# Kernel optimization log

Hardware: AMD Instinct MI355X
Metric: run time of the kernel (lower is better)

The kernel has to match this reference:

```python
import math
import jax, jax.numpy as jnp
import numpy as np

B, NPC, K, D, T, L = 512, 32, 12, 64, 64, 4  # crystals, atoms/crystal, knn, node_dim, time_dim, layers
N = B * NPC
E_IN = 2 * D + 1 + T   # 193
N_IN = 2 * D + T       # 192


def setup_inputs() -> dict:
    key = jax.random.key(0)
    ks = jax.random.split(key, 32)
    rn = lambda k, shp, s=0.05: jax.random.normal(k, shp, jnp.float32) * s
    inp = {}
    inp["z_nodes"] = jax.random.normal(ks[0], (N, 128), jnp.float32)
    inp["t"] = jax.random.uniform(ks[1], (B,), jnp.float32) * 1000.0
    inp["frac_coords"] = jax.random.uniform(ks[2], (N, 3), jnp.float32)
    inp["lattice"] = jnp.eye(3, dtype=jnp.float32) * 5.0 + rn(ks[3], (B, 3, 3), 0.3)
    inp["batch_indices"] = jnp.repeat(jnp.arange(B, dtype=jnp.int32), NPC)
    inp["num_atoms"] = NPC
    # time_mlp: Linear(T, 2T) -> SiLU -> Linear(2T, T)
    inp["time_w1"] = rn(ks[4], (T, 2 * T)); inp["time_b1"] = rn(ks[5], (2 * T,))
    inp["time_w2"] = rn(ks[6], (2 * T, T)); inp["time_b2"] = rn(ks[7], (T,))
    # node_embedding: Linear(128, D)
    inp["emb_w"] = rn(ks[8], (128, D)); inp["emb_b"] = rn(ks[9], (D,))
    # per-layer EGNN params stacked on leading L axis
    inp["edge_w1"] = rn(ks[10], (L, E_IN, D)); inp["edge_b1"] = rn(ks[11], (L, D))
    inp["edge_w2"] = rn(ks[12], (L, D, D));    inp["edge_b2"] = rn(ks[13], (L, D))
    inp["coord_w1"] = rn(ks[14], (L, D, D));   inp["coord_b1"] = rn(ks[15], (L, D))
    inp["coord_w2"] = rn(ks[16], (L, D, 1))
    inp["node_w1"] = rn(ks[17], (L, N_IN, D)); inp["node_b1"] = rn(ks[18], (L, D))
    inp["node_w2"] = rn(ks[19], (L, D, D));    inp["node_b2"] = rn(ks[20], (L, D))
    return inp


def _forward(z_nodes, t, frac_coords, lattice, batch_indices, num_atoms,
             time_w1, time_b1, time_w2, time_b2, emb_w, emb_b,
             edge_w1, edge_b1, edge_w2, edge_b2, coord_w1, coord_b1, coord_w2,
             node_w1, node_b1, node_w2, node_b2):
    silu = jax.nn.silu
    n = num_atoms
    b = lattice.shape[0]
    n_nodes = z_nodes.shape[0]

    # ---- time embedding ----
    half = T // 2
    freqs = jnp.exp(jnp.arange(half, dtype=jnp.float32) * (-math.log(10000.0) / (half - 1)))
    ang = t[:, None] * freqs[None, :]
    sinu = jnp.concatenate([jnp.sin(ang), jnp.cos(ang)], axis=-1)  # [B, T]
    t_feat = silu(sinu @ time_w1 + time_b1) @ time_w2 + time_b2     # [B, T]
    t_nodes = t_feat[batch_indices]                                  # [N, T]

    h = z_nodes @ emb_w + emb_b                                      # [N, D]

    # ---- vectorized PBC KNN graph (all crystals have n atoms) ----
    f = frac_coords.reshape(b, n, 3)
    diff_f = f[:, :, None, :] - f[:, None, :, :]
    diff_f = diff_f - jnp.round(diff_f)
    diff_c = jnp.einsum('bijk,bkl->bijl', diff_f, lattice)           # [b,n,n,3]
    dist_sq = jnp.sum(diff_c * diff_c, axis=-1)                      # [b,n,n]
    dist_sq = jnp.where(jnp.eye(n, dtype=bool)[None], jnp.inf, dist_sq)
    k = min(K, n - 1)
    _, idx = jax.lax.top_k(-dist_sq, k)                              # [b,n,k] neighbor indices
    offs = (jnp.arange(b, dtype=jnp.int32) * n)[:, None, None]
    edge_src = (idx + offs).reshape(-1)                              # neighbors j
    edge_dst = (jnp.broadcast_to(jnp.arange(n, dtype=jnp.int32)[None, :, None], (b, n, k)) + offs).reshape(-1)
    diff_cart = jnp.take_along_axis(diff_c, jnp.broadcast_to(idx[..., None], (b, n, k, 3)), axis=2).reshape(-1, 3)
    dist_sq_e = jnp.take_along_axis(dist_sq, idx, axis=2).reshape(-1, 1)

    t_edges = t_nodes[edge_src]                                      # [E, T]

    total_shift = jnp.zeros((n_nodes, 3), dtype=h.dtype)
    for l in range(L):
        edge_in = jnp.concatenate([h[edge_src], h[edge_dst], dist_sq_e, t_edges], axis=-1)
        m = silu(edge_in @ edge_w1[l] + edge_b1[l])
        m = silu(m @ edge_w2[l] + edge_b2[l])                        # [E, D]
        cw = silu(m @ coord_w1[l] + coord_b1[l]) @ coord_w2[l]       # [E, 1]
        coord_update = jax.ops.segment_sum(diff_cart * cw, edge_src, num_segments=n_nodes)
        m_i = jax.ops.segment_sum(m, edge_dst, num_segments=n_nodes)
        node_in = jnp.concatenate([h, m_i, t_nodes], axis=-1)
        h = h + (silu(node_in @ node_w1[l] + node_b1[l]) @ node_w2[l] + node_b2[l])
        total_shift = total_shift + coord_update

    inv_lat = jnp.linalg.inv(lattice)[batch_indices]                 # [N,3,3]
    shift_frac = jnp.einsum('ni,nij->nj', total_shift, inv_lat)
    return shift_frac, h


def reference(z_nodes, t, frac_coords, lattice, batch_indices, num_atoms,
              time_w1, time_b1, time_w2, time_b2, emb_w, emb_b,
              edge_w1, edge_b1, edge_w2, edge_b2, coord_w1, coord_b1, coord_w2,
              node_w1, node_b1, node_w2, node_b2):
    return _forward(z_nodes, t, frac_coords, lattice, batch_indices, num_atoms,
                    time_w1, time_b1, time_w2, time_b2, emb_w, emb_b,
                    edge_w1, edge_b1, edge_w2, edge_b2, coord_w1, coord_b1, coord_w2,
                    node_w1, node_b1, node_w2, node_b2)
```

## Files before the change

### kernel.cpp

```cpp
#include <hip/hip_runtime.h>
#include <hip/hip_bf16.h>
#include <math.h>

#define NB 512
#define NPC 32
#define KNN 12
#define NL 4
#define NN (NB*NPC)
#define WPL 28672

typedef float v4f __attribute__((ext_vector_type(4)));
typedef short s8v __attribute__((ext_vector_type(8)));

__device__ __forceinline__ float silu_f(float x) {
    return x * __builtin_amdgcn_rcpf(1.0f + __builtin_amdgcn_exp2f(x * -1.44269504088896341f));
}

__device__ __forceinline__ unsigned short f2bf(float x) {
    unsigned u = __float_as_uint(x);
    u += 0x7fffu + ((u >> 16) & 1u);
    return (unsigned short)(u >> 16);
}

__device__ __forceinline__ unsigned pk2bf(float a, float b) {
    __hip_bfloat162 t = __float22bfloat162_rn(make_float2(a, b));
    union { __hip_bfloat162 h; unsigned u; } c; c.h = t;
    return c.u;
}

__device__ __forceinline__ int div12(int e) { return (e * 1366) >> 14; }

template<int R>
__device__ __forceinline__ void gemm_acc(const float* A, int astride,
                                         const float* __restrict__ Wg,
                                         int K, int lane, float* acc) {
#pragma unroll 2
    for (int kq = 0; kq < (K >> 2); ++kq) {
        float w0 = Wg[(4*kq+0)*64 + lane];
        float w1 = Wg[(4*kq+1)*64 + lane];
        float w2 = Wg[(4*kq+2)*64 + lane];
        float w3 = Wg[(4*kq+3)*64 + lane];
#pragma unroll
        for (int r = 0; r < R; ++r) {
            float4 a = *(const float4*)(A + r*astride + 4*kq);
            acc[r] = fmaf(a.x, w0, acc[r]);
            acc[r] = fmaf(a.y, w1, acc[r]);
            acc[r] = fmaf(a.z, w2, acc[r]);
            acc[r] = fmaf(a.w, w3, acc[r]);
        }
    }
}

extern "C" __global__ void prepack_w(const float* __restrict__ edge_w1, const float* __restrict__ edge_w2,
                                     const float* __restrict__ coord_w1, const float* __restrict__ node_w1,
                                     const float* __restrict__ node_w2, unsigned short* __restrict__ wout) {
    int g = blockIdx.x * 256 + threadIdx.x;
    if (g >= 4 * WPL / 8) return;
    int l = (g * 8) / WPL;
    int r = (g * 8) % WPL;
    int base, nKt, mat;
    if      (r < 8192)  { base = 0;     nKt = 2; mat = 0; }
    else if (r < 12288) { base = 8192;  nKt = 2; mat = 1; }
    else if (r < 16384) { base = 12288; nKt = 2; mat = 2; }
    else if (r < 24576) { base = 16384; nKt = 4; mat = 3; }
    else                { base = 24576; nKt = 2; mat = 4; }
    int idx = r - base;
    int lane = (idx >> 3) & 63, t = idx >> 9;
    int kt = t % nKt, nt = t / nKt;
    int k0 = kt*32 + ((lane >> 4) & 3)*8;
    int n  = nt*16 + (lane & 15);
    unsigned short o[8];
#pragma unroll
    for (int j = 0; j < 8; ++j) {
        int k = k0 + j;
        float v;
        if      (mat == 0) v = (n < 64) ? edge_w1[l*193*64 + k*64 + n] : edge_w1[l*193*64 + (64+k)*64 + (n-64)];
        else if (mat == 1) v = edge_w2 [l*4096 + k*64 + n];
        else if (mat == 2) v = coord_w1[l*4096 + k*64 + n];
        else if (mat == 3) v = node_w1 [l*192*64 + k*64 + n];
        else               v = node_w2 [l*4096 + k*64 + n];
        o[j] = f2bf(v);
    }
    *(s8v*)(wout + g*8) = *(s8v*)o;
}

extern "C" __global__ __launch_bounds__(512, 2)
void crystal_fused(const float* __restrict__ z_nodes, const float* __restrict__ t_in,
                   const float* __restrict__ frac,    const float* __restrict__ lattice,
                   const float* __restrict__ time_w1, const float* __restrict__ time_b1,
                   const float* __restrict__ time_w2, const float* __restrict__ time_b2,
                   const float* __restrict__ emb_w,   const float* __restrict__ emb_b,
                   const float* __restrict__ edge_w1, const float* __restrict__ edge_b1,
                   const float* __restrict__ edge_b2, const float* __restrict__ coord_b1,
                   const float* __restrict__ coord_w2,
                   const float* __restrict__ node_w1, const float* __restrict__ node_b1,
                   const float* __restrict__ node_b2,
                   const unsigned short* __restrict__ wbf,
                   float* __restrict__ out)
{
    __shared__ __align__(16) float s_h[32*65];
    __shared__ __align__(16) unsigned short s_habf[32*136];
    __shared__ __align__(16) unsigned short s_n1bf[32*72];
    __shared__ __align__(16) float s_hs[32*68];
    __shared__ __align__(16) float s_hd[32*68];
    __shared__ __align__(16) unsigned short s_tiles16[8*1152];
    __shared__ float s_dsq[32][33];
    __shared__ float2 s_emeta[384];
    __shared__ float s_endc[384*3];
    __shared__ float s_frac[32][3];
    __shared__ float s_lat[9], s_inv[9];
    __shared__ float s_sinu[64], s_t1[128], s_tf[64];
    __shared__ float s_tb4[NL*64], s_nb4[NL*64];
    __shared__ float s_shift[32*3];

    const int tid  = threadIdx.x;
    const int c    = blockIdx.x;
    const int lane = tid & 63;
    const int wave = tid >> 6;
    const int q4   = lane >> 4;
    const int c16  = lane & 15;
    const int base = c * NPC;

    if (tid < 96) {
        ((float*)s_frac)[tid] = frac[base*3 + tid];
    } else if (tid < 105) {
        s_lat[tid-96] = lattice[c*9 + (tid-96)];
    } else if (tid >= 128 && tid < 160) {
        int i = tid - 128;
        float freq = expf((float)i * (-9.210340371976184f / 31.0f));
        float ang  = t_in[c] * freq;
        s_sinu[i]    = sinf(ang);
        s_sinu[i+32] = cosf(ang);
    }
    __syncthreads();

    float* dcf = (float*)s_tiles16;
    {
        float l00=s_lat[0],l01=s_lat[1],l02=s_lat[2];
        float l10=s_lat[3],l11=s_lat[4],l12=s_lat[5];
        float l20=s_lat[6],l21=s_lat[7],l22=s_lat[8];
        for (int p = tid; p < 1024; p += 512) {
            int i = p >> 5, j = p & 31;
            float dx = s_frac[i][0]-s_frac[j][0];
            float dy = s_frac[i][1]-s_frac[j][1];
            float dz = s_frac[i][2]-s_frac[j][2];
            dx -= rintf(dx); dy -= rintf(dy); dz -= rintf(dz);
            float cx = dx*l00 + dy*l10 + dz*l20;
            float cy = dx*l01 + dy*l11 + dz*l21;
            float cz = dx*l02 + dy*l12 + dz*l22;
            float dd = cx*cx + cy*cy + cz*cz;
            s_dsq[i][j] = (i==j) ? 3.0e38f : dd;
            dcf[p*3+0]=cx; dcf[p*3+1]=cy; dcf[p*3+2]=cz;
        }
    }
    __syncthreads();

    if (tid < 32) {
        int i = tid;
        for (int k = 0; k < KNN; ++k) {
            float best = 3.9e38f; int bj = 0;
            for (int j = 0; j < 32; ++j) {
                float v = s_dsq[i][j];
                if (v < best) { best = v; bj = j; }
            }
            s_dsq[i][bj] = 3.9e38f;
            int e = i*KNN + k;
            s_emeta[e] = make_float2(best, __int_as_float(bj));
            int p = (i<<5) + bj;
            s_endc[e*3+0] = dcf[p*3+0];
            s_endc[e*3+1] = dcf[p*3+1];
            s_endc[e*3+2] = dcf[p*3+2];
        }
    } else if (tid >= 128 && tid < 256) {
        int jj = tid - 128;
        float p0 = time_b1[jj], p1=0.f, p2=0.f, p3=0.f;
        for (int k = 0; k < 64; k += 4) {
            p0 = fmaf(s_sinu[k+0], time_w1[(k+0)*128+jj], p0);
            p1 = fmaf(s_sinu[k+1], time_w1[(k+1)*128+jj], p1);
            p2 = fmaf(s_sinu[k+2], time_w1[(k+2)*128+jj], p2);
            p3 = fmaf(s_sinu[k+3], time_w1[(k+3)*128+jj], p3);
        }
        s_t1[jj] = silu_f((p0+p1) + (p2+p3));
    }
    __syncthreads();

    if (tid < 64) {
        float p0=time_b2[tid],p1=0.f,p2=0.f,p3=0.f;
        for (int k = 0; k < 128; k += 4) {
            p0 = fmaf(s_t1[k+0], time_w2[(k+0)*64+tid], p0);
            p1 = fmaf(s_t1[k+1], time_w2[(k+1)*64+tid], p1);
            p2 = fmaf(s_t1[k+2], time_w2[(k+2)*64+tid], p2);
            p3 = fmaf(s_t1[k+3], time_w2[(k+3)*64+tid], p3);
        }
        s_tf[tid] = (p0+p1) + (p2+p3);
    } else if (tid < 160) {
        s_shift[tid-64] = 0.0f;
    }
    __syncthreads();

    float* zbuf = (float*)s_tiles16;
    for (int q = tid; q < 4096; q += 512) zbuf[q] = z_nodes[base*128 + q];
    {
        int l = wave >> 1, kind = wave & 1;
        const float* Wt = kind ? (node_w1 + l*192*64 + 128*64) : (edge_w1 + l*193*64 + 129*64);
        const float* bb = kind ? (node_b1 + l*64) : (edge_b1 + l*64);
        float p0 = bb[lane], p1=0.f, p2=0.f, p3=0.f;
        for (int k = 0; k < 64; k += 4) {
            p0 = fmaf(s_tf[k+0], Wt[(k+0)*64 + lane], p0);
            p1 = fmaf(s_tf[k+1], Wt[(k+1)*64 + lane], p1);
            p2 = fmaf(s_tf[k+2], Wt[(k+2)*64 + lane], p2);
            p3 = fmaf(s_tf[k+3], Wt[(k+3)*64 + lane], p3);
        }
        float v = (p0+p1) + (p2+p3);
        if (kind) s_nb4[l*64 + lane] = v;
        else      s_tb4[l*64 + lane] = v;
    }
    __syncthreads();

    {
        float acc[4];
#pragma unroll
        for (int r = 0; r < 4; ++r) acc[r] = emb_b[lane];
        gemm_acc<4>(zbuf + (wave*4)*128, 128, emb_w, 128, lane, acc);
#pragma unroll
        for (int r = 0; r < 4; ++r) {
            int row = wave*4 + r;
            s_h[row*65 + lane] = acc[r];
            s_habf[row*136 + lane] = f2bf(acc[r]);
        }
    }
    __syncthreads();

    for (int l = 0; l < NL; ++l) {
        const unsigned short* wl = wbf + l*WPL;
        const float* w1row = edge_w1 + l*193*64 + 128*64;
        float b2e_v[4], cb1_v[4], w2c_v[4];
#pragma unroll
        for (int nt = 0; nt < 4; ++nt) {
            b2e_v[nt] = edge_b2 [l*64 + nt*16 + c16];
            cb1_v[nt] = coord_b1[l*64 + nt*16 + c16];
            w2c_v[nt] = coord_w2[l*64 + nt*16 + c16];
        }

        {
            s8v a[2][2];
#pragma unroll
            for (int mt = 0; mt < 2; ++mt)
#pragma unroll
                for (int kt = 0; kt < 2; ++kt)
                    a[mt][kt] = *(const s8v*)(s_habf + (mt*16 + c16)*136 + kt*32 + q4*8);
            v4f acc[2] = {{0.f,0.f,0.f,0.f},{0.f,0.f,0.f,0.f}};
#pragma unroll
            for (int kt = 0; kt < 2; ++kt) {
                s8v b = *(const s8v*)(wl + ((wave*2+kt)*64 + lane)*8);
#pragma unroll
                for (int mt = 0; mt < 2; ++mt)
                    acc[mt] = __builtin_amdgcn_mfma_f32_16x16x32_bf16(a[mt][kt], b, acc[mt], 0, 0, 0);
            }
            int col = wave*16 + c16;
            if (wave < 4) {
#pragma unroll
                for (int mt = 0; mt < 2; ++mt)
#pragma unroll
                    for (int reg = 0; reg < 4; ++reg)
                        s_hs[(mt*16 + q4*4 + reg)*68 + col] = acc[mt][reg];
            } else {
                int colb = col - 64;
                float tbv = s_tb4[l*64 + colb];
#pragma unroll
                for (int mt = 0; mt < 2; ++mt)
#pragma unroll
                    for (int reg = 0; reg < 4; ++reg)
                        s_hd[(mt*16 + q4*4 + reg)*68 + colb] = acc[mt][reg] + tbv;
            }
        }
        __syncthreads();

        {
            s8v w2f[8], wc1f[8];
#pragma unroll
            for (int nt = 0; nt < 4; ++nt)
#pragma unroll
                for (int kt = 0; kt < 2; ++kt) {
                    w2f [nt*2+kt] = *(const s8v*)(wl +  8192 + ((nt*2+kt)*64 + lane)*8);
                    wc1f[nt*2+kt] = *(const s8v*)(wl + 12288 + ((nt*2+kt)*64 + lane)*8);
                }
            union F4 { float4 v; float f[4]; };
            F4 W4[4];
            W4[0].v = *(const float4*)(w1row + q4*8);
            W4[1].v = *(const float4*)(w1row + q4*8 + 4);
            W4[2].v = *(const float4*)(w1row + 32 + q4*8);
            W4[3].v = *(const float4*)(w1row + 32 + q4*8 + 4);

            unsigned short* tile = s_tiles16 + wave*1152;
            float miacc[4][4];
#pragma unroll
            for (int a2 = 0; a2 < 4; ++a2)
#pragma unroll
                for (int b2 = 0; b2 < 4; ++b2) miacc[a2][b2] = 0.f;

            float2 me0 = s_emeta[wave*48 +  0 + c16];
            float2 me1 = s_emeta[wave*48 + 16 + c16];
            float2 me2 = s_emeta[wave*48 + 32 + c16];

            F4 H[4], G[4];
            {
                int srcn = __float_as_int(me0.y);
                int dstn = div12(wave*48 + c16);
                const float* hsr = s_hs + srcn*68 + q4*8;
                const float* hdr = s_hd + dstn*68 + q4*8;
                H[0].v = *(const float4*)(hsr);      H[1].v = *(const float4*)(hsr+4);
                H[2].v = *(const float4*)(hsr+32);   H[3].v = *(const float4*)(hsr+36);
                G[0].v = *(const float4*)(hdr);      G[1].v = *(const float4*)(hdr+4);
                G[2].v = *(const float4*)(hdr+32);   G[3].v = *(const float4*)(hdr+36);
            }

#pragma unroll
            for (int m = 0; m < 3; ++m) {
                const int e0g = wave*48 + m*16;
                const float dq = (m==0) ? me0.x : (m==1) ? me1.x : me2.x;
                union S8 { s8v v; unsigned u[4]; } A0, A1;
#pragma unroll
                for (int g2 = 0; g2 < 4; ++g2) {
                    float s0 = silu_f(fmaf(dq, W4[g2].f[0], H[g2].f[0] + G[g2].f[0]));
                    float s1 = silu_f(fmaf(dq, W4[g2].f[1], H[g2].f[1] + G[g2].f[1]));
                    float s2 = silu_f(fmaf(dq, W4[g2].f[2], H[g2].f[2] + G[g2].f[2]));
                    float s3 = silu_f(fmaf(dq, W4[g2].f[3], H[g2].f[3] + G[g2].f[3]));
                    unsigned lo = pk2bf(s0, s1), hi2 = pk2bf(s2, s3);
                    if (g2 < 2) { A0.u[g2*2] = lo; A0.u[g2*2+1] = hi2; }
                    else        { A1.u[(g2-2)*2] = lo; A1.u[(g2-2)*2+1] = hi2; }
                }
                if (m < 2) {
                    float2 men = (m==0) ? me1 : me2;
                    int srcn = __float_as_int(men.y);
                    int dstn = div12(e0g + 16 + c16);
                    const float* hsr = s_hs + srcn*68 + q4*8;
                    const float* hdr = s_hd + dstn*68 + q4*8;
                    H[0].v = *(const float4*)(hsr);      H[1].v = *(const float4*)(hsr+4);
                    H[2].v = *(const float4*)(hsr+32);   H[3].v = *(const float4*)(hsr+36);
                    G[0].v = *(const float4*)(hdr);      G[1].v = *(const float4*)(hdr+4);
                    G[2].v = *(const float4*)(hdr+32);   G[3].v = *(const float4*)(hdr+36);
                }

                const int thr = (m==0) ? 3 : (m==1) ? 2 : 1;
                const int dlo = m;
#pragma unroll
                for (int nt = 0; nt < 4; ++nt) {
                    v4f acc = {0.f,0.f,0.f,0.f};
                    acc = __builtin_amdgcn_mfma_f32_16x16x32_bf16(A0.v, w2f[nt*2+0], acc, 0,0,0);
                    acc = __builtin_amdgcn_mfma_f32_16x16x32_bf16(A1.v, w2f[nt*2+1], acc, 0,0,0);
                    int col = nt*16 + c16;
                    float msum = 0.f;
#pragma unroll
                    for (int reg = 0; reg < 4; ++reg) {
                        float v = silu_f(acc[reg] + b2e_v[nt]);
                        tile[(q4*4 + reg)*72 + col] = f2bf(v);
                        msum += v;
                    }
                    bool hi = (q4 >= thr);
                    miacc[nt][dlo]   += hi ? 0.f : msum;
                    miacc[nt][dlo+1] += hi ? msum : 0.f;
                }
                asm volatile("s_waitcnt lgkmcnt(0)" ::: "memory");
                s8v c0 = *(const s8v*)(tile + c16*72 +      q4*8);
                s8v c1 = *(const s8v*)(tile + c16*72 + 32 + q4*8);
                float cwp[4] = {0.f,0.f,0.f,0.f};
#pragma unroll
                for (int nt = 0; nt < 4; ++nt) {
                    v4f acc = {0.f,0.f,0.f,0.f};
                    acc = __builtin_amdgcn_mfma_f32_16x16x32_bf16(c0, wc1f[nt*2+0], acc, 0,0,0);
                    acc = __builtin_amdgcn_mfma_f32_16x16x32_bf16(c1, wc1f[nt*2+1], acc, 0,0,0);
#pragma unroll
                    for (int reg = 0; reg < 4; ++reg)
                        cwp[reg] += silu_f(acc[reg] + cb1_v[nt]) * w2c_v[nt];
                }
#pragma unroll
                for (int reg = 0; reg < 4; ++reg) {
                    float v = cwp[reg];
                    v += __shfl_xor(v, 1); v += __shfl_xor(v, 2);
                    v += __shfl_xor(v, 4); v += __shfl_xor(v, 8);
                    int e = e0g + q4*4 + reg;
                    if (c16 < 3) {
                        int src = __float_as_int(s_emeta[e].y);
                        atomicAdd(&s_shift[src*3 + c16], s_endc[e*3 + c16] * v);
                    }
                }
            }
#pragma unroll
            for (int nt = 0; nt < 4; ++nt)
#pragma unroll
                for (int d = 0; d < 4; ++d) {
                    float v = miacc[nt][d];
                    v += __shfl_xor(v, 16);
                    v += __shfl_xor(v, 32);
                    s_habf[(wave*4 + d)*136 + 64 + nt*16 + c16] = f2bf(v);
                }
        }

        const int ntA = wave >> 1, mtA = wave & 1;
        s8v bn1[4];
#pragma unroll
        for (int kt = 0; kt < 4; ++kt)
            bn1[kt] = *(const s8v*)(wl + 16384 + ((ntA*4+kt)*64 + lane)*8);
        __syncthreads();

        {
            int col = ntA*16 + c16;
            float nbc = s_nb4[l*64 + col];
            v4f acc = {0.f,0.f,0.f,0.f};
#pragma unroll
            for (int kt = 0; kt < 4; ++kt) {
                s8v a = *(const s8v*)(s_habf + (mtA*16 + c16)*136 + kt*32 + q4*8);
                acc = __builtin_amdgcn_mfma_f32_16x16x32_bf16(a, bn1[kt], acc, 0,0,0);
            }
#pragma unroll
            for (int reg = 0; reg < 4; ++reg) {
                int row = mtA*16 + q4*4 + reg;
                s_n1bf[row*72 + col] = f2bf(silu_f(acc[reg] + nbc));
            }
        }
        s8v bn20 = *(const s8v*)(wl + 24576 + ((ntA*2+0)*64 + lane)*8);
        s8v bn21 = *(const s8v*)(wl + 24576 + ((ntA*2+1)*64 + lane)*8);
        __syncthreads();

        {
            int col = ntA*16 + c16;
            float nb2_v = node_b2[l*64 + col];
            s8v a0 = *(const s8v*)(s_n1bf + (mtA*16 + c16)*72 +      q4*8);
            s8v a1 = *(const s8v*)(s_n1bf + (mtA*16 + c16)*72 + 32 + q4*8);
            v4f acc = {0.f,0.f,0.f,0.f};
            acc = __builtin_amdgcn_mfma_f32_16x16x32_bf16(a0, bn20, acc, 0,0,0);
            acc = __builtin_amdgcn_mfma_f32_16x16x32_bf16(a1, bn21, acc, 0,0,0);
#pragma unroll
            for (int reg = 0; reg < 4; ++reg) {
                int row = mtA*16 + q4*4 + reg;
                float hn = s_h[row*65 + col] + acc[reg] + nb2_v;
                s_h[row*65 + col] = hn;
                s_habf[row*136 + col] = f2bf(hn);
            }
        }
        __syncthreads();
    }

    if (tid == 0) {
        float a=s_lat[0],b=s_lat[1],cc=s_lat[2];
        float d=s_lat[3],e=s_lat[4],f =s_lat[5];
        float g=s_lat[6],h2=s_lat[7],i2=s_lat[8];
        float A  =  (e*i2 - f*h2);
        float Bm = -(d*i2 - f*g);
        float C  =  (d*h2 - e*g);
        float det = a*A + b*Bm + cc*C;
        float rd = 1.0f/det;
        s_inv[0] = A*rd;
        s_inv[1] = -(b*i2 - cc*h2)*rd;
        s_inv[2] =  (b*f  - cc*e )*rd;
        s_inv[3] = Bm*rd;
        s_inv[4] =  (a*i2 - cc*g )*rd;
        s_inv[5] = -(a*f  - cc*d )*rd;
        s_inv[6] = C*rd;
        s_inv[7] = -(a*h2 - b*g  )*rd;
        s_inv[8] =  (a*e  - b*d  )*rd;
    }
    __syncthreads();
    if (tid < 96) {
        int r = tid/3, j = tid%3;
        float v = s_shift[r*3+0]*s_inv[0*3+j]
                + s_shift[r*3+1]*s_inv[1*3+j]
                + s_shift[r*3+2]*s_inv[2*3+j];
        out[(base + r)*3 + j] = v;
    }
    for (int q = tid; q < 2048; q += 512) {
        int row = q >> 6, colq = q & 63;
        out[NN*3 + base*64 + q] = s_h[row*65 + colq];
    }
}

extern "C" void kernel_launch(void* const* d_in, const int* in_sizes, int n_in,
                              void* d_out, int out_size, void* d_ws, size_t ws_size,
                              hipStream_t stream) {
    unsigned short* wbf = (unsigned short*)d_ws;
    prepack_w<<<(4*WPL/8 + 255)/256, 256, 0, stream>>>(
        (const float*)d_in[12], (const float*)d_in[14], (const float*)d_in[16],
        (const float*)d_in[19], (const float*)d_in[21], wbf);
    crystal_fused<<<NB, 512, 0, stream>>>(
        (const float*)d_in[0],  (const float*)d_in[1],  (const float*)d_in[2],  (const float*)d_in[3],
        (const float*)d_in[6],  (const float*)d_in[7],  (const float*)d_in[8],  (const float*)d_in[9],
        (const float*)d_in[10], (const float*)d_in[11],
        (const float*)d_in[12], (const float*)d_in[13], (const float*)d_in[15],
        (const float*)d_in[17], (const float*)d_in[18],
        (const float*)d_in[19], (const float*)d_in[20], (const float*)d_in[22],
        wbf, (float*)d_out);
}
```

Measured before the change: 211.5 us.

## Halve block to 256 threads, doubling per-wave work across all stages

New measurement: 200.7 us. 5.1% less time.

```diff
diff --git a/kernel.cpp b/kernel.cpp
--- a/kernel.cpp
+++ b/kernel.cpp
@@ -84,7 +84,7 @@
     *(s8v*)(wout + g*8) = *(s8v*)o;
 }
 
-extern "C" __global__ __launch_bounds__(512, 2)
+extern "C" __global__ __launch_bounds__(256, 2)
 void crystal_fused(const float* __restrict__ z_nodes, const float* __restrict__ t_in,
                    const float* __restrict__ frac,    const float* __restrict__ lattice,
                    const float* __restrict__ time_w1, const float* __restrict__ time_b1,
@@ -103,7 +103,7 @@
     __shared__ __align__(16) unsigned short s_n1bf[32*72];
     __shared__ __align__(16) float s_hs[32*68];
     __shared__ __align__(16) float s_hd[32*68];
-    __shared__ __align__(16) unsigned short s_tiles16[8*1152];
+    __shared__ __align__(16) unsigned short s_tiles16[8192];
     __shared__ float s_dsq[32][33];
     __shared__ float2 s_emeta[384];
     __shared__ float s_endc[384*3];
@@ -139,7 +139,7 @@
         float l00=s_lat[0],l01=s_lat[1],l02=s_lat[2];
         float l10=s_lat[3],l11=s_lat[4],l12=s_lat[5];
         float l20=s_lat[6],l21=s_lat[7],l22=s_lat[8];
-        for (int p = tid; p < 1024; p += 512) {
+        for (int p = tid; p < 1024; p += 256) {
             int i = p >> 5, j = p & 31;
             float dx = s_frac[i][0]-s_frac[j][0];
             float dy = s_frac[i][1]-s_frac[j][1];
@@ -171,7 +171,7 @@
             s_endc[e*3+1] = dcf[p*3+1];
             s_endc[e*3+2] = dcf[p*3+2];
         }
-    } else if (tid >= 128 && tid < 256) {
+    } else if (tid >= 128) {
         int jj = tid - 128;
         float p0 = time_b1[jj], p1=0.f, p2=0.f, p3=0.f;
         for (int k = 0; k < 64; k += 4) {
@@ -199,11 +199,13 @@
     __syncthreads();
 
     float* zbuf = (float*)s_tiles16;
-    for (int q = tid; q < 4096; q += 512) zbuf[q] = z_nodes[base*128 + q];
-    {
-        int l = wave >> 1, kind = wave & 1;
-        const float* Wt = kind ? (node_w1 + l*192*64 + 128*64) : (edge_w1 + l*193*64 + 129*64);
-        const float* bb = kind ? (node_b1 + l*64) : (edge_b1 + l*64);
+    for (int q = tid; q < 4096; q += 256) zbuf[q] = z_nodes[base*128 + q];
+#pragma unroll
+    for (int it = 0; it < 2; ++it) {
+        int t = wave + it*4;
+        int lt = t >> 1, kind = t & 1;
+        const float* Wt = kind ? (node_w1 + lt*192*64 + 128*64) : (edge_w1 + lt*193*64 + 129*64);
+        const float* bb = kind ? (node_b1 + lt*64) : (edge_b1 + lt*64);
         float p0 = bb[lane], p1=0.f, p2=0.f, p3=0.f;
         for (int k = 0; k < 64; k += 4) {
             p0 = fmaf(s_tf[k+0], Wt[(k+0)*64 + lane], p0);
@@ -212,19 +214,19 @@
             p3 = fmaf(s_tf[k+3], Wt[(k+3)*64 + lane], p3);
         }
         float v = (p0+p1) + (p2+p3);
-        if (kind) s_nb4[l*64 + lane] = v;
-        else      s_tb4[l*64 + lane] = v;
+        if (kind) s_nb4[lt*64 + lane] = v;
+        else      s_tb4[lt*64 + lane] = v;
     }
     __syncthreads();
 
     {
-        float acc[4];
-#pragma unroll
-        for (int r = 0; r < 4; ++r) acc[r] = emb_b[lane];
-        gemm_acc<4>(zbuf + (wave*4)*128, 128, emb_w, 128, lane, acc);
-#pragma unroll
-        for (int r = 0; r < 4; ++r) {
-            int row = wave*4 + r;
+        float acc[8];
+#pragma unroll
+        for (int r = 0; r < 8; ++r) acc[r] = emb_b[lane];
+        gemm_acc<8>(zbuf + (wave*8)*128, 128, emb_w, 128, lane, acc);
+#pragma unroll
+        for (int r = 0; r < 8; ++r) {
+            int row = wave*8 + r;
             s_h[row*65 + lane] = acc[r];
             s_habf[row*136 + lane] = f2bf(acc[r]);
         }
@@ -249,30 +251,28 @@
 #pragma unroll
                 for (int kt = 0; kt < 2; ++kt)
                     a[mt][kt] = *(const s8v*)(s_habf + (mt*16 + c16)*136 + kt*32 + q4*8);
-            v4f acc[2] = {{0.f,0.f,0.f,0.f},{0.f,0.f,0.f,0.f}};
+            v4f accS[2] = {{0.f,0.f,0.f,0.f},{0.f,0.f,0.f,0.f}};
+            v4f accD[2] = {{0.f,0.f,0.f,0.f},{0.f,0.f,0.f,0.f}};
 #pragma unroll
             for (int kt = 0; kt < 2; ++kt) {
-                s8v b = *(const s8v*)(wl + ((wave*2+kt)*64 + lane)*8);
-#pragma unroll
-                for (int mt = 0; mt < 2; ++mt)
-                    acc[mt] = __builtin_amdgcn_mfma_f32_16x16x32_bf16(a[mt][kt], b, acc[mt], 0, 0, 0);
+                s8v bS = *(const s8v*)(wl + ((wave*2+kt)*64 + lane)*8);
+                s8v bD = *(const s8v*)(wl + (((wave+4)*2+kt)*64 + lane)*8);
+#pragma unroll
+                for (int mt = 0; mt < 2; ++mt) {
+                    accS[mt] = __builtin_amdgcn_mfma_f32_16x16x32_bf16(a[mt][kt], bS, accS[mt], 0, 0, 0);
+                    accD[mt] = __builtin_amdgcn_mfma_f32_16x16x32_bf16(a[mt][kt], bD, accD[mt], 0, 0, 0);
+                }
             }
             int col = wave*16 + c16;
-            if (wave < 4) {
-#pragma unroll
-                for (int mt = 0; mt < 2; ++mt)
-#pragma unroll
-                    for (int reg = 0; reg < 4; ++reg)
-                        s_hs[(mt*16 + q4*4 + reg)*68 + col] = acc[mt][reg];
-            } else {
-                int colb = col - 64;
-                float tbv = s_tb4[l*64 + colb];
-#pragma unroll
-                for (int mt = 0; mt < 2; ++mt)
-#pragma unroll
-                    for (int reg = 0; reg < 4; ++reg)
-                        s_hd[(mt*16 + q4*4 + reg)*68 + colb] = acc[mt][reg] + tbv;
-            }
+            float tbv = s_tb4[l*64 + col];
+#pragma unroll
+            for (int mt = 0; mt < 2; ++mt)
+#pragma unroll
+                for (int reg = 0; reg < 4; ++reg) {
+                    int row = mt*16 + q4*4 + reg;
+                    s_hs[row*68 + col] = accS[mt][reg];
+                    s_hd[row*68 + col] = accD[mt][reg] + tbv;
+                }
         }
         __syncthreads();
 
@@ -293,20 +293,33 @@
             W4[3].v = *(const float4*)(w1row + 32 + q4*8 + 4);
 
             unsigned short* tile = s_tiles16 + wave*1152;
-            float miacc[4][4];
-#pragma unroll
-            for (int a2 = 0; a2 < 4; ++a2)
-#pragma unroll
-                for (int b2 = 0; b2 < 4; ++b2) miacc[a2][b2] = 0.f;
-
-            float2 me0 = s_emeta[wave*48 +  0 + c16];
-            float2 me1 = s_emeta[wave*48 + 16 + c16];
-            float2 me2 = s_emeta[wave*48 + 32 + c16];
+            float miacc[4][2];
+#pragma unroll
+            for (int a2 = 0; a2 < 4; ++a2) { miacc[a2][0] = 0.f; miacc[a2][1] = 0.f; }
+
+            auto flushd = [&](int d) {
+                int s = d & 1;
+#pragma unroll
+                for (int nt = 0; nt < 4; ++nt) {
+                    float v = miacc[nt][s];
+                    v += __shfl_xor(v, 16);
+                    v += __shfl_xor(v, 32);
+                    s_habf[(wave*8 + d)*136 + 64 + nt*16 + c16] = f2bf(v);
+                    miacc[nt][s] = 0.f;
+                }
+            };
+
+            float2 me0 = s_emeta[wave*96 +  0 + c16];
+            float2 me1 = s_emeta[wave*96 + 16 + c16];
+            float2 me2 = s_emeta[wave*96 + 32 + c16];
+            float2 me3 = s_emeta[wave*96 + 48 + c16];
+            float2 me4 = s_emeta[wave*96 + 64 + c16];
+            float2 me5 = s_emeta[wave*96 + 80 + c16];
 
             F4 H[4], G[4];
             {
                 int srcn = __float_as_int(me0.y);
-                int dstn = div12(wave*48 + c16);
+                int dstn = div12(wave*96 + c16);
                 const float* hsr = s_hs + srcn*68 + q4*8;
                 const float* hdr = s_hd + dstn*68 + q4*8;
                 H[0].v = *(const float4*)(hsr);      H[1].v = *(const float4*)(hsr+4);
@@ -316,9 +329,10 @@
             }
 
 #pragma unroll
-            for (int m = 0; m < 3; ++m) {
-                const int e0g = wave*48 + m*16;
-                const float dq = (m==0) ? me0.x : (m==1) ? me1.x : me2.x;
+            for (int m = 0; m < 6; ++m) {
+                const int e0g = wave*96 + m*16;
+                const float dq = (m==0) ? me0.x : (m==1) ? me1.x : (m==2) ? me2.x
+                               : (m==3) ? me3.x : (m==4) ? me4.x : me5.x;
                 union S8 { s8v v; unsigned u[4]; } A0, A1;
 #pragma unroll
                 for (int g2 = 0; g2 < 4; ++g2) {
@@ -330,8 +344,9 @@
                     if (g2 < 2) { A0.u[g2*2] = lo; A0.u[g2*2+1] = hi2; }
                     else        { A1.u[(g2-2)*2] = lo; A1.u[(g2-2)*2+1] = hi2; }
                 }
-                if (m < 2) {
-                    float2 men = (m==0) ? me1 : me2;
+                if (m < 5) {
+                    float2 men = (m==0) ? me1 : (m==1) ? me2 : (m==2) ? me3
+                               : (m==3) ? me4 : me5;
                     int srcn = __float_as_int(men.y);
                     int dstn = div12(e0g + 16 + c16);
                     const float* hsr = s_hs + srcn*68 + q4*8;
@@ -342,8 +357,9 @@
                     G[2].v = *(const float4*)(hdr+32);   G[3].v = *(const float4*)(hdr+36);
                 }
 
-                const int thr = (m==0) ? 3 : (m==1) ? 2 : 1;
-                const int dlo = m;
+                const int dlo = (m < 3) ? m : m + 1;
+                const int thr = 3 - (m % 3);
+                const int slo = dlo & 1;
 #pragma unroll
                 for (int nt = 0; nt < 4; ++nt) {
                     v4f acc = {0.f,0.f,0.f,0.f};
@@ -358,8 +374,8 @@
                         msum += v;
                     }
                     bool hi = (q4 >= thr);
-                    miacc[nt][dlo]   += hi ? 0.f : msum;
-                    miacc[nt][dlo+1] += hi ? msum : 0.f;
+                    miacc[nt][slo]     += hi ? 0.f : msum;
+                    miacc[nt][slo ^ 1] += hi ? msum : 0.f;
                 }
                 asm volatile("s_waitcnt lgkmcnt(0)" ::: "memory");
                 s8v c0 = *(const s8v*)(tile + c16*72 +      q4*8);
@@ -385,58 +401,70 @@
                         atomicAdd(&s_shift[src*3 + c16], s_endc[e*3 + c16] * v);
                     }
                 }
+                if (m == 0) { flushd(0); }
+                else if (m == 1) { flushd(1); }
+                else if (m == 2) { flushd(2); flushd(3); }
+                else if (m == 3) { flushd(4); }
+                else if (m == 4) { flushd(5); }
+                else             { flushd(6); flushd(7); }
             }
-#pragma unroll
-            for (int nt = 0; nt < 4; ++nt)
-#pragma unroll
-                for (int d = 0; d < 4; ++d) {
-                    float v = miacc[nt][d];
-                    v += __shfl_xor(v, 16);
-                    v += __shfl_xor(v, 32);
-                    s_habf[(wave*4 + d)*136 + 64 + nt*16 + c16] = f2bf(v);
-                }
-        }
-
-        const int ntA = wave >> 1, mtA = wave & 1;
-        s8v bn1[4];
-#pragma unroll
-        for (int kt = 0; kt < 4; ++kt)
-            bn1[kt] = *(const s8v*)(wl + 16384 + ((ntA*4+kt)*64 + lane)*8);
+        }
+
+        const int mtA = wave & 1, nt0 = wave >> 1, nt1 = (wave >> 1) + 2;
+        s8v bn1[8];
+#pragma unroll
+        for (int kt = 0; kt < 4; ++kt) {
+            bn1[kt]   = *(const s8v*)(wl + 16384 + ((nt0*4+kt)*64 + lane)*8);
+            bn1[4+kt] = *(const s8v*)(wl + 16384 + ((nt1*4+kt)*64 + lane)*8);
+        }
         __syncthreads();
 
         {
-            int col = ntA*16 + c16;
-            float nbc = s_nb4[l*64 + col];
-            v4f acc = {0.f,0.f,0.f,0.f};
-#pragma unroll
-            for (int kt = 0; kt < 4; ++kt) {
-                s8v a = *(const s8v*)(s_habf + (mtA*16 + c16)*136 + kt*32 + q4*8);
-                acc = __builtin_amdgcn_mfma_f32_16x16x32_bf16(a, bn1[kt], acc, 0,0,0);
+            s8v aA[4];
+#pragma unroll
+            for (int kt = 0; kt < 4; ++kt)
+                aA[kt] = *(const s8v*)(s_habf + (mtA*16 + c16)*136 + kt*32 + q4*8);
+#pragma unroll
+            for (int it = 0; it < 2; ++it) {
+                int nt = it ? nt1 : nt0;
+                int col = nt*16 + c16;
+                float nbc = s_nb4[l*64 + col];
+                v4f acc = {0.f,0.f,0.f,0.f};
+#pragma unroll
+                for (int kt = 0; kt < 4; ++kt)
+                    acc = __builtin_amdgcn_mfma_f32_16x16x32_bf16(aA[kt], bn1[it*4+kt], acc, 0,0,0);
+#pragma unroll
+                for (int reg = 0; reg < 4; ++reg) {
+                    int row = mtA*16 + q4*4 + reg;
+                    s_n1bf[row*72 + col] = f2bf(silu_f(acc[reg] + nbc));
+                }
             }
-#pragma unroll
-            for (int reg = 0; reg < 4; ++reg) {
-                int row = mtA*16 + q4*4 + reg;
-                s_n1bf[row*72 + col] = f2bf(silu_f(acc[reg] + nbc));
-            }
-        }
-        s8v bn20 = *(const s8v*)(wl + 24576 + ((ntA*2+0)*64 + lane)*8);
-        s8v bn21 = *(const s8v*)(wl + 24576 + ((ntA*2+1)*64 + lane)*8);
+        }
+        s8v bn2[4];
+        bn2[0] = *(const s8v*)(wl + 24576 + ((nt0*2+0)*64 + lane)*8);
+        bn2[1] = *(const s8v*)(wl + 24576 + ((nt0*2+1)*64 + lane)*8);
+        bn2[2] = *(const s8v*)(wl + 24576 + ((nt1*2+0)*64 + lane)*8);
+        bn2[3] = *(const s8v*)(wl + 24576 + ((nt1*2+1)*64 + lane)*8);
         __syncthreads();
 
         {
-            int col = ntA*16 + c16;
-            float nb2_v = node_b2[l*64 + col];
             s8v a0 = *(const s8v*)(s_n1bf + (mtA*16 + c16)*72 +      q4*8);
             s8v a1 = *(const s8v*)(s_n1bf + (mtA*16 + c16)*72 + 32 + q4*8);
-            v4f acc = {0.f,0.f,0.f,0.f};
-            acc = __builtin_amdgcn_mfma_f32_16x16x32_bf16(a0, bn20, acc, 0,0,0);
-            acc = __builtin_amdgcn_mfma_f32_16x16x32_bf16(a1, bn21, acc, 0,0,0);
-#pragma unroll
-            for (int reg = 0; reg < 4; ++reg) {
-                int row = mtA*16 + q4*4 + reg;
-                float hn = s_h[row*65 + col] + acc[reg] + nb2_v;
-                s_h[row*65 + col] = hn;
-                s_habf[row*136 + col] = f2bf(hn);
+#pragma unroll
+            for (int it = 0; it < 2; ++it) {
+                int nt = it ? nt1 : nt0;
+                int col = nt*16 + c16;
+                float nb2_v = node_b2[l*64 + col];
+                v4f acc = {0.f,0.f,0.f,0.f};
+                acc = __builtin_amdgcn_mfma_f32_16x16x32_bf16(a0, bn2[it*2+0], acc, 0,0,0);
+                acc = __builtin_amdgcn_mfma_f32_16x16x32_bf16(a1, bn2[it*2+1], acc, 0,0,0);
+#pragma unroll
+                for (int reg = 0; reg < 4; ++reg) {
+                    int row = mtA*16 + q4*4 + reg;
+                    float hn = s_h[row*65 + col] + acc[reg] + nb2_v;
+                    s_h[row*65 + col] = hn;
+                    s_habf[row*136 + col] = f2bf(hn);
+                }
             }
         }
         __syncthreads();
@@ -469,7 +497,7 @@
                 + s_shift[r*3+2]*s_inv[2*3+j];
         out[(base + r)*3 + j] = v;
     }
-    for (int q = tid; q < 2048; q += 512) {
+    for (int q = tid; q < 2048; q += 256) {
         int row = q >> 6, colq = q & 63;
         out[NN*3 + base*64 + q] = s_h[row*65 + colq];
     }
@@ -482,7 +510,7 @@
     prepack_w<<<(4*WPL/8 + 255)/256, 256, 0, stream>>>(
         (const float*)d_in[12], (const float*)d_in[14], (const float*)d_in[16],
         (const float*)d_in[19], (const float*)d_in[21], wbf);
-    crystal_fused<<<NB, 512, 0, stream>>>(
+    crystal_fused<<<NB, 256, 0, stream>>>(
         (const float*)d_in[0],  (const float*)d_in[1],  (const float*)d_in[2],  (const float*)d_in[3],
         (const float*)d_in[6],  (const float*)d_in[7],  (const float*)d_in[8],  (const float*)d_in[9],
         (const float*)d_in[10], (const float*)d_in[11],
```
